# Performance work log

Hardware: AMD Instinct MI355X
Metric: run time of the kernel (lower is better)

## Reference

```python
import jax, jax.numpy as jnp
import numpy as np

EPS = 1e-6
THRESHOLD = 0.5


def ternarize(weight):
    # absmax scale along last dim (in_features)
    scale = jnp.clip(jnp.max(jnp.abs(weight), axis=-1, keepdims=True), EPS, None)
    normalized = weight / scale
    ternary = jnp.where(normalized > THRESHOLD, 1.0,
                        jnp.where(normalized < -THRESHOLD, -1.0, 0.0)).astype(weight.dtype)
    return ternary * scale


def setup_inputs() -> dict:
    key = jax.random.key(0)
    k1, k2, k3 = jax.random.split(key, 3)
    B, S, D_in, D_out = 4, 4096, 2048, 2048
    x = jax.random.normal(k1, (B, S, D_in), dtype=jnp.float32)
    # kaiming-uniform-ish init
    bound_w = (6.0 / D_in) ** 0.5 / (1.0 + 5.0) ** 0.5
    weight = jax.random.uniform(k2, (D_out, D_in), dtype=jnp.float32, minval=-bound_w, maxval=bound_w)
    bound_b = 1.0 / D_in ** 0.5
    bias = jax.random.uniform(k3, (D_out,), dtype=jnp.float32, minval=-bound_b, maxval=bound_b)
    return {"x": x, "weight": weight, "bias": bias}


def reference(x, weight, bias):
    qw = ternarize(weight)  # [out, in]
    # F.linear: x @ qw.T + bias
    return jnp.einsum('bsi,oi->bso', x, qw) + bias
```

## Files before the change

kernel.cpp:

```cpp
#include <hip/hip_runtime.h>
#include <hip/hip_bf16.h>
#include <stdint.h>


#define M_DIM 16384
#define N_DIM 2048
#define K_DIM 2048

#define BM 256
#define BN 256
#define BK 64
#define NT (K_DIM / BK)

typedef __bf16 bf16x8 __attribute__((ext_vector_type(8)));
typedef float f32x4 __attribute__((ext_vector_type(4)));

__global__ __launch_bounds__(256) void cvt_x_k(
    const float* __restrict__ x, __hip_bfloat16* __restrict__ xb) {
  const size_t i = ((size_t)blockIdx.x * 256 + threadIdx.x) * 8;
  const float4 a = *(const float4*)(x + i);
  const float4 b = *(const float4*)(x + i + 4);
  bf16x8 o;
  o[0] = (__bf16)a.x; o[1] = (__bf16)a.y; o[2] = (__bf16)a.z; o[3] = (__bf16)a.w;
  o[4] = (__bf16)b.x; o[5] = (__bf16)b.y; o[6] = (__bf16)b.z; o[7] = (__bf16)b.w;
  *(bf16x8*)((__bf16*)xb + i) = o;
}

__global__ __launch_bounds__(256) void ternarize_k(
    const float* __restrict__ w,
    __hip_bfloat16* __restrict__ qw,
    float* __restrict__ scales) {
  const int row = blockIdx.x;
  const float* wr = w + (size_t)row * K_DIM;

  float m = 0.0f;
  for (int k = threadIdx.x; k < K_DIM; k += 256)
    m = fmaxf(m, fabsf(wr[k]));

  for (int off = 32; off > 0; off >>= 1)
    m = fmaxf(m, __shfl_down(m, off, 64));
  __shared__ float wmax[4];
  if ((threadIdx.x & 63) == 0) wmax[threadIdx.x >> 6] = m;
  __syncthreads();
  float scale = fmaxf(fmaxf(wmax[0], wmax[1]), fmaxf(wmax[2], wmax[3]));
  scale = fmaxf(scale, 1e-6f);
  if (threadIdx.x == 0) scales[row] = scale;

  for (int k = threadIdx.x; k < K_DIM; k += 256) {
    const float v = wr[k] / scale;
    const float t = (v > 0.5f) ? 1.0f : ((v < -0.5f) ? -1.0f : 0.0f);
    qw[(size_t)row * K_DIM + k] = __float2bfloat16(t);
  }
}

static __device__ __forceinline__ void gload16(const __hip_bfloat16* g,
                                               char* l) {
  __builtin_amdgcn_global_load_lds(
      (__attribute__((address_space(1))) void*)const_cast<__hip_bfloat16*>(g),
      (__attribute__((address_space(3))) void*)(l), 16, 0, 0);
}

#define MFMA_(d, a, b) \
  d = __builtin_amdgcn_mfma_f32_16x16x32_bf16(a, b, d, 0, 0, 0)

#define SBAR()  __builtin_amdgcn_s_barrier()
#define SCHED() __builtin_amdgcn_sched_barrier(0)
#define CFENCE() asm volatile("" ::: "memory")

__global__ __launch_bounds__(512, 2) void gemm_bt_k(
    const __hip_bfloat16* __restrict__ A,
    const __hip_bfloat16* __restrict__ B,
    const float* __restrict__ scales,
    const float* __restrict__ bias,
    float* __restrict__ C) {
  __shared__ __align__(128) char lds[131072];

  const int tid  = threadIdx.x;
  const int wave = tid >> 6;
  const int lane = tid & 63;
  const int quad = lane >> 4;
  const int lrow = lane & 15;
  const int wr = wave >> 2;
  const int wc = wave & 3;

  const int orig = blockIdx.x;
  const int wg = (orig & 7) * 64 + (orig >> 3);
  const int bx = wg & 7;
  const int by = wg >> 3;
  const int m0 = by * BM;
  const int n0 = bx * BN;

  const int srow  = tid >> 3;
  const int scol8 = (tid & 7) ^ (srow & 7);
  const __hip_bfloat16* Ag = A + (size_t)(m0 + srow) * K_DIM + scol8 * 8;
  const __hip_bfloat16* Bg = B + (size_t)(n0 + srow) * K_DIM + scol8 * 8;
  const int sbase = wave * 1024;

  const int axor = lrow & 7;
  const int cs0 = ((0 + quad) ^ axor) * 16;
  const int cs1 = ((4 + quad) ^ axor) * 16;
  const int aHalf = wr * 16384;
  const int bHalf = 32768 + (wc >> 1) * 16384;
  const int bRow  = (wc & 1) * 64 + lrow;
  const int oA0 = aHalf + lrow * 128 + cs0;
  const int oA1 = aHalf + lrow * 128 + cs1;
  const int oB0 = bHalf + bRow * 128 + cs0;
  const int oB1 = bHalf + bRow * 128 + cs1;

  auto STAGE_A = [&](int dst, int kk) {
    const __hip_bfloat16* g = Ag + kk;
    gload16(g,               lds + dst);
    gload16(g +  64 * K_DIM, lds + dst + 8192);
    gload16(g + 128 * K_DIM, lds + dst + 16384);
    gload16(g + 192 * K_DIM, lds + dst + 24576);
  };
  auto STAGE_B = [&](int dst, int kk) {
    const __hip_bfloat16* g = Bg + kk;
    gload16(g,               lds + dst + 32768);
    gload16(g +  64 * K_DIM, lds + dst + 40960);
    gload16(g + 128 * K_DIM, lds + dst + 49152);
    gload16(g + 192 * K_DIM, lds + dst + 57344);
  };

  f32x4 acc[8][4] = {};

  STAGE_A(sbase, 0);          STAGE_B(sbase, 0);
  STAGE_A(sbase + 65536, BK); STAGE_B(sbase + 65536, BK);
  asm volatile("s_waitcnt vmcnt(8)" ::: "memory");
  SBAR();

  for (int t = 0; t < NT; ++t) {
    const int bo  = (t & 1) << 16;
    const int kk2 = (t + 2) * BK;
    const bool pf = (t + 2) < NT;
    const int aB0 = bo + oA0, aB1 = bo + oA1;
    const int bB0 = bo + oB0, bB1 = bo + oB1;

    bf16x8 af0[4][2], af1[4][2], bf0[2][2], bf1[2][2];

#pragma unroll
    for (int m = 0; m < 4; ++m) {
      af0[m][0] = *(const bf16x8*)(lds + aB0 + m * 2048);
      af0[m][1] = *(const bf16x8*)(lds + aB1 + m * 2048);
    }
#pragma unroll
    for (int n = 0; n < 2; ++n) {
      bf0[n][0] = *(const bf16x8*)(lds + bB0 + n * 2048);
      bf0[n][1] = *(const bf16x8*)(lds + bB1 + n * 2048);
    }
    __builtin_amdgcn_s_setprio(1);
#pragma unroll
    for (int m = 0; m < 4; ++m)
#pragma unroll
      for (int n = 0; n < 2; ++n) {
        MFMA_(acc[m][n], af0[m][0], bf0[n][0]);
        MFMA_(acc[m][n], af0[m][1], bf0[n][1]);
      }
    __builtin_amdgcn_s_setprio(0);

#pragma unroll
    for (int m = 0; m < 4; ++m) {
      af1[m][0] = *(const bf16x8*)(lds + aB0 + (m + 4) * 2048);
      af1[m][1] = *(const bf16x8*)(lds + aB1 + (m + 4) * 2048);
    }
    __builtin_amdgcn_s_setprio(1);
#pragma unroll
    for (int m = 0; m < 4; ++m)
#pragma unroll
      for (int n = 0; n < 2; ++n) {
        MFMA_(acc[m + 4][n], af1[m][0], bf0[n][0]);
        MFMA_(acc[m + 4][n], af1[m][1], bf0[n][1]);
      }
    __builtin_amdgcn_s_setprio(0);

    SCHED();
    CFENCE();
    SBAR();
    SCHED();

    if (pf) STAGE_A(bo + sbase, kk2);
#pragma unroll
    for (int n = 0; n < 2; ++n) {
      bf1[n][0] = *(const bf16x8*)(lds + bB0 + (n + 2) * 2048);
      bf1[n][1] = *(const bf16x8*)(lds + bB1 + (n + 2) * 2048);
    }
    __builtin_amdgcn_s_setprio(1);
#pragma unroll
    for (int m = 0; m < 4; ++m)
#pragma unroll
      for (int n = 0; n < 2; ++n) {
        MFMA_(acc[m + 4][n + 2], af1[m][0], bf1[n][0]);
        MFMA_(acc[m + 4][n + 2], af1[m][1], bf1[n][1]);
      }
    __builtin_amdgcn_s_setprio(0);

    SCHED();
    CFENCE();
    SBAR();
    SCHED();

    if (pf) STAGE_B(bo + sbase, kk2);
    __builtin_amdgcn_s_setprio(1);
#pragma unroll
    for (int m = 0; m < 4; ++m)
#pragma unroll
      for (int n = 0; n < 2; ++n) {
        MFMA_(acc[m][n + 2], af0[m][0], bf1[n][0]);
        MFMA_(acc[m][n + 2], af0[m][1], bf1[n][1]);
      }
    __builtin_amdgcn_s_setprio(0);

    if (t < NT - 2)
      asm volatile("s_waitcnt vmcnt(8)" ::: "memory");
    else
      asm volatile("s_waitcnt vmcnt(0)" ::: "memory");
    SBAR();
  }

#pragma unroll
  for (int n = 0; n < 4; ++n) {
    const int col = n0 + wc * 64 + n * 16 + lrow;
    const float s = scales[col];
    const float b = bias[col];
#pragma unroll
    for (int m = 0; m < 8; ++m) {
      const int rbase = m0 + wr * 128 + m * 16 + quad * 4;
#pragma unroll
      for (int r = 0; r < 4; ++r)
        C[(size_t)(rbase + r) * N_DIM + col] = acc[m][n][r] * s + b;
    }
  }
}

extern "C" void kernel_launch(void* const* d_in, const int* in_sizes, int n_in,
                              void* d_out, int out_size, void* d_ws, size_t ws_size,
                              hipStream_t stream) {
  const float* x    = (const float*)d_in[0];
  const float* w    = (const float*)d_in[1];
  const float* bias = (const float*)d_in[2];
  float* out = (float*)d_out;

  __hip_bfloat16* xb = (__hip_bfloat16*)d_ws;
  __hip_bfloat16* qw = (__hip_bfloat16*)((char*)d_ws + (size_t)M_DIM * K_DIM * 2);
  float* scales = (float*)((char*)d_ws + (size_t)M_DIM * K_DIM * 2 + (size_t)N_DIM * K_DIM * 2);

  cvt_x_k<<<dim3((M_DIM * (size_t)K_DIM) / (256 * 8)), dim3(256), 0, stream>>>(x, xb);
  ternarize_k<<<dim3(N_DIM), dim3(256), 0, stream>>>(w, qw, scales);
  gemm_bt_k<<<dim3((M_DIM / BM) * (N_DIM / BN)), dim3(512), 0, stream>>>(xb, qw, scales, bias, out);
}
```

Before: 355.3 us.

## Software-pipeline LDS fragment loads across K iterations in GEMM main loop

Restructures the GEMM inner loop so the A and B fragments for the next K tile are read from LDS during the current tile's MFMA phases. Loads are split and interleaved with the MFMA groups, and the barriers and waitcnt points are reordered so the global-to-LDS prefetches of B then A are issued at new places. The aim is to hide LDS read latency behind matrix math. In exchange it holds more live fragment registers, which could cause register spills or lower occupancy, and the hand-tuned waitcnt counts carry a correctness risk.

Result: no change. 352.8 us (-0.7%).

```diff
diff --git a/kernel.cpp b/kernel.cpp
--- a/kernel.cpp
+++ b/kernel.cpp
@@ -65,7 +65,6 @@
 
 #define SBAR()  __builtin_amdgcn_s_barrier()
 #define SCHED() __builtin_amdgcn_sched_barrier(0)
-#define CFENCE() asm volatile("" ::: "memory")
 
 __global__ __launch_bounds__(512, 2) void gemm_bt_k(
     const __hip_bfloat16* __restrict__ A,
@@ -123,31 +122,41 @@
   };
 
   f32x4 acc[8][4] = {};
+  bf16x8 af0[4][2], af1[4][2], bf0[2][2], bf0n[2][2], bf1[2][2];
 
   STAGE_A(sbase, 0);          STAGE_B(sbase, 0);
   STAGE_A(sbase + 65536, BK); STAGE_B(sbase + 65536, BK);
   asm volatile("s_waitcnt vmcnt(8)" ::: "memory");
   SBAR();
+#pragma unroll
+  for (int m = 0; m < 4; ++m) {
+    af0[m][0] = *(const bf16x8*)(lds + oA0 + m * 2048);
+    af0[m][1] = *(const bf16x8*)(lds + oA1 + m * 2048);
+  }
+#pragma unroll
+  for (int n = 0; n < 2; ++n) {
+    bf0[n][0] = *(const bf16x8*)(lds + oB0 + n * 2048);
+    bf0[n][1] = *(const bf16x8*)(lds + oB1 + n * 2048);
+  }
 
   for (int t = 0; t < NT; ++t) {
     const int bo  = (t & 1) << 16;
+    const int nbo = bo ^ 65536;
     const int kk2 = (t + 2) * BK;
     const bool pf = (t + 2) < NT;
-    const int aB0 = bo + oA0, aB1 = bo + oA1;
-    const int bB0 = bo + oB0, bB1 = bo + oB1;
-
-    bf16x8 af0[4][2], af1[4][2], bf0[2][2], bf1[2][2];
-
-#pragma unroll
-    for (int m = 0; m < 4; ++m) {
-      af0[m][0] = *(const bf16x8*)(lds + aB0 + m * 2048);
-      af0[m][1] = *(const bf16x8*)(lds + aB1 + m * 2048);
-    }
+
 #pragma unroll
     for (int n = 0; n < 2; ++n) {
-      bf0[n][0] = *(const bf16x8*)(lds + bB0 + n * 2048);
-      bf0[n][1] = *(const bf16x8*)(lds + bB1 + n * 2048);
-    }
+      bf1[n][0] = *(const bf16x8*)(lds + bo + oB0 + (n + 2) * 2048);
+      bf1[n][1] = *(const bf16x8*)(lds + bo + oB1 + (n + 2) * 2048);
+    }
+    SCHED();
+#pragma unroll
+    for (int m = 0; m < 2; ++m) {
+      af1[m][0] = *(const bf16x8*)(lds + bo + oA0 + (m + 4) * 2048);
+      af1[m][1] = *(const bf16x8*)(lds + bo + oA1 + (m + 4) * 2048);
+    }
+    SCHED();
     __builtin_amdgcn_s_setprio(1);
 #pragma unroll
     for (int m = 0; m < 4; ++m)
@@ -157,12 +166,59 @@
         MFMA_(acc[m][n], af0[m][1], bf0[n][1]);
       }
     __builtin_amdgcn_s_setprio(0);
-
+    SCHED();
+
+#pragma unroll
+    for (int m = 2; m < 4; ++m) {
+      af1[m][0] = *(const bf16x8*)(lds + bo + oA0 + (m + 4) * 2048);
+      af1[m][1] = *(const bf16x8*)(lds + bo + oA1 + (m + 4) * 2048);
+    }
+    SCHED();
+    asm volatile("s_waitcnt lgkmcnt(8)" ::: "memory");
+    SBAR();
+    if (pf) STAGE_B(bo + sbase, kk2);
+    SCHED();
+    __builtin_amdgcn_s_setprio(1);
+#pragma unroll
+    for (int m = 0; m < 4; ++m)
+#pragma unroll
+      for (int n = 0; n < 2; ++n) {
+        MFMA_(acc[m][n + 2], af0[m][0], bf1[n][0]);
+        MFMA_(acc[m][n + 2], af0[m][1], bf1[n][1]);
+      }
+    __builtin_amdgcn_s_setprio(0);
+    SCHED();
+
+    if (pf)
+      asm volatile("s_waitcnt vmcnt(4)" ::: "memory");
+    else
+      asm volatile("s_waitcnt vmcnt(0)" ::: "memory");
+    asm volatile("s_waitcnt lgkmcnt(0)" ::: "memory");
+    SBAR();
+    if (pf) STAGE_A(bo + sbase, kk2);
 #pragma unroll
     for (int m = 0; m < 4; ++m) {
-      af1[m][0] = *(const bf16x8*)(lds + aB0 + (m + 4) * 2048);
-      af1[m][1] = *(const bf16x8*)(lds + aB1 + (m + 4) * 2048);
-    }
+      af0[m][0] = *(const bf16x8*)(lds + nbo + oA0 + m * 2048);
+      af0[m][1] = *(const bf16x8*)(lds + nbo + oA1 + m * 2048);
+    }
+    SCHED();
+    __builtin_amdgcn_s_setprio(1);
+#pragma unroll
+    for (int m = 0; m < 4; ++m)
+#pragma unroll
+      for (int n = 0; n < 2; ++n) {
+        MFMA_(acc[m + 4][n + 2], af1[m][0], bf1[n][0]);
+        MFMA_(acc[m + 4][n + 2], af1[m][1], bf1[n][1]);
+      }
+    __builtin_amdgcn_s_setprio(0);
+    SCHED();
+
+#pragma unroll
+    for (int n = 0; n < 2; ++n) {
+      bf0n[n][0] = *(const bf16x8*)(lds + nbo + oB0 + n * 2048);
+      bf0n[n][1] = *(const bf16x8*)(lds + nbo + oB1 + n * 2048);
+    }
+    SCHED();
     __builtin_amdgcn_s_setprio(1);
 #pragma unroll
     for (int m = 0; m < 4; ++m)
@@ -172,49 +228,12 @@
         MFMA_(acc[m + 4][n], af1[m][1], bf0[n][1]);
       }
     __builtin_amdgcn_s_setprio(0);
-
-    SCHED();
-    CFENCE();
-    SBAR();
-    SCHED();
-
-    if (pf) STAGE_A(bo + sbase, kk2);
+    SCHED();
 #pragma unroll
     for (int n = 0; n < 2; ++n) {
-      bf1[n][0] = *(const bf16x8*)(lds + bB0 + (n + 2) * 2048);
-      bf1[n][1] = *(const bf16x8*)(lds + bB1 + (n + 2) * 2048);
-    }
-    __builtin_amdgcn_s_setprio(1);
-#pragma unroll
-    for (int m = 0; m < 4; ++m)
-#pragma unroll
-      for (int n = 0; n < 2; ++n) {
-        MFMA_(acc[m + 4][n + 2], af1[m][0], bf1[n][0]);
-        MFMA_(acc[m + 4][n + 2], af1[m][1], bf1[n][1]);
-      }
-    __builtin_amdgcn_s_setprio(0);
-
-    SCHED();
-    CFENCE();
-    SBAR();
-    SCHED();
-
-    if (pf) STAGE_B(bo + sbase, kk2);
-    __builtin_amdgcn_s_setprio(1);
-#pragma unroll
-    for (int m = 0; m < 4; ++m)
-#pragma unroll
-      for (int n = 0; n < 2; ++n) {
-        MFMA_(acc[m][n + 2], af0[m][0], bf1[n][0]);
-        MFMA_(acc[m][n + 2], af0[m][1], bf1[n][1]);
-      }
-    __builtin_amdgcn_s_setprio(0);
-
-    if (t < NT - 2)
-      asm volatile("s_waitcnt vmcnt(8)" ::: "memory");
-    else
-      asm volatile("s_waitcnt vmcnt(0)" ::: "memory");
-    SBAR();
+      bf0[n][0] = bf0n[n][0];
+      bf0[n][1] = bf0n[n][1];
+    }
   }
 
 #pragma unroll
```
